# Kernel tuning notes

Measured on AMD Instinct MI355X. Metric: run time of the kernel, lower is better.

The kernel has to match this reference:

```python
import jax, jax.numpy as jnp
import numpy as np

TAU = 32.0


def setup_inputs() -> dict:
    key = jax.random.key(0)
    k1, k2, k3, k4, k5 = jax.random.split(key, 5)
    B, IN, E, D, M = 32768, 768, 256, 9, 10
    feature = jax.random.normal(k1, (B, IN), dtype=jnp.float32)
    category = jax.random.randint(k2, (B,), 0, D)  # unused in forward math
    # nn.Linear(input_dim, emb_dim, bias=False) stores weight [emb_dim, input_dim]
    W_topic = jax.random.normal(k3, (E, IN), dtype=jnp.float32) * (1.0 / np.sqrt(IN))
    W_domain = jax.random.normal(k4, (E, IN), dtype=jnp.float32) * (1.0 / np.sqrt(IN))
    memory = jax.random.normal(k5, (D, M, E), dtype=jnp.float32)  # stacked domain memory banks
    return {"feature": feature, "category": category, "W_topic": W_topic,
            "W_domain": W_domain, "memory": memory}


def reference(feature, category, W_topic, W_domain, memory):
    # L2-normalize features along dim 1
    f = feature / jnp.linalg.norm(feature, axis=1, keepdims=True)
    topic = f @ W_topic.T      # [B, E]
    dom = f @ W_domain.T       # [B, E]
    # per-domain memory attention, batched over all D domains at once
    att = jax.nn.softmax(jnp.einsum('be,dme->bdm', topic, memory) * TAU, axis=-1)  # [B, D, M]
    sep = jnp.einsum('bdm,dme->bde', att, memory)                                   # [B, D, E]
    domain_att = jnp.einsum('bde,be->bd', sep, dom)                                 # [B, D]
    return jax.nn.softmax(domain_att * TAU, axis=1)[:, None, :]                     # [B, 1, D]
```

## Files before the change

kernel.cpp:

```cpp
#include <hip/hip_runtime.h>
#include <math.h>

typedef __attribute__((ext_vector_type(8))) short short8;
typedef __attribute__((ext_vector_type(4))) float f32x4;
typedef __attribute__((ext_vector_type(4))) unsigned short u16x4;

#define TAUF 32.0f

constexpr int NT     = 24;
constexpr int BUF_SZ = 40960;
constexpr int A_HI   = 0;
constexpr int A_LO   = 8192;
constexpr int B_HI   = 16384;
constexpr int B_LO   = 28672;
constexpr int CSTR   = 196;

__global__ __launch_bounds__(256) void precompute_pr(
    const float* __restrict__ Wt, const float* __restrict__ Wd,
    const float* __restrict__ mem, unsigned short* __restrict__ PRhi,
    unsigned short* __restrict__ PRlo) {
  int blk = blockIdx.x, t = threadIdx.x;
  if (blk >= 180) {
    for (int p = 0; p < 3; ++p) {
      PRhi[blk * 768 + t + p * 256] = 0;
      PRlo[blk * 768 + t + p * 256] = 0;
    }
    return;
  }
  __shared__ float mlds[256];
  const float* W = (blk >= 90) ? Wd : Wt;
  int dm = (blk >= 90) ? blk - 90 : blk;
  mlds[t] = mem[dm * 256 + t];
  __syncthreads();
  for (int p = 0; p < 3; ++p) {
    int i = t + p * 256;
    float acc = 0.f;
    #pragma unroll 8
    for (int e = 0; e < 256; ++e) acc += mlds[e] * W[e * 768 + i];
    unsigned int b = __float_as_uint(acc);
    unsigned short hi = (unsigned short)(b >> 16);
    float hf = __uint_as_float(b & 0xffff0000u);
    unsigned short lo = (unsigned short)(__float_as_uint(acc - hf) >> 16);
    PRhi[blk * 768 + i] = hi;
    PRlo[blk * 768 + i] = lo;
  }
}

__global__ __launch_bounds__(512, 1) void fused_mfma(
    const float* __restrict__ feat, const unsigned short* __restrict__ PRhi,
    const unsigned short* __restrict__ PRlo, float* __restrict__ out) {
  __shared__ f32x4 smemv[6400];
  __shared__ float invn[128];
  __shared__ float sarr[1152];
  char* smem = (char*)smemv;

  const int t    = threadIdx.x;
  const int lane = t & 63;
  const int wid  = t >> 6;
  const int rg   = wid >> 1;
  const int cg   = wid & 1;
  const int b0   = blockIdx.x * 128;

  const int ar0 = t >> 3;
  const int aq  = t & 7;
  const float* gA0 = feat + (size_t)(b0 + ar0) * 768 + aq * 4;
  const float* gA1 = gA0 + (size_t)64 * 768;
  const int aw0 = ar0 * 64 + aq * 8;
  const int aw1 = (ar0 + 64) * 64 + aq * 8;

  const int iid = wid * 3;

  const int laneA = ((lane & 15) << 6) | ((lane >> 4) << 4);

  f32x4 acc0[6], acc1[6];
  #pragma unroll
  for (int j = 0; j < 6; ++j) {
    acc0[j] = (f32x4){0.f, 0.f, 0.f, 0.f};
    acc1[j] = (f32x4){0.f, 0.f, 0.f, 0.f};
  }
  float ssq0 = 0.f, ssq1 = 0.f;

  auto issueB = [&](int kt, int bb) {
    #pragma unroll
    for (int u = 0; u < 3; ++u) {
      int i  = iid + u;
      int pl = i / 12;
      int idx = i - pl * 12;
      int G  = idx * 64 + lane;
      const unsigned short* basep = pl ? PRlo : PRhi;
      const char* g = (const char*)basep + (G >> 2) * 1536 + kt * 64 + (G & 3) * 16;
      char* l = smem + bb * BUF_SZ + (pl ? B_LO : B_HI) + idx * 1024;
      __builtin_amdgcn_global_load_lds((const unsigned int*)g, (unsigned int*)l,
                                       16, 0, 0);
    }
  };

  auto cvtwrite = [&](float4 v, char* dhi, char* dlo, float& ssq) {
    ssq += v.x * v.x + v.y * v.y + v.z * v.z + v.w * v.w;
    float xs[4] = {v.x, v.y, v.z, v.w};
    u16x4 hi, lo;
    #pragma unroll
    for (int e = 0; e < 4; ++e) {
      float x = xs[e];
      unsigned int bu = __float_as_uint(x);
      hi[e] = (unsigned short)(bu >> 16);
      float hf = __uint_as_float(bu & 0xffff0000u);
      lo[e] = (unsigned short)(__float_as_uint(x - hf) >> 16);
    }
    *(u16x4*)dhi = hi;
    *(u16x4*)dlo = lo;
  };

  auto domfma = [&](int bb) {
    char* base = smem + bb * BUF_SZ;
    const int aoff = rg * 2048 + laneA;
    short8 ah0 = *(const short8*)(base + A_HI + aoff);
    short8 ah1 = *(const short8*)(base + A_HI + aoff + 1024);
    short8 al0 = *(const short8*)(base + A_LO + aoff);
    short8 al1 = *(const short8*)(base + A_LO + aoff + 1024);
    const int boff = cg * 6144 + laneA;
    #pragma unroll
    for (int j = 0; j < 6; ++j) {
      short8 bh = *(const short8*)(base + B_HI + boff + j * 1024);
      short8 bl = *(const short8*)(base + B_LO + boff + j * 1024);
      acc0[j] = __builtin_amdgcn_mfma_f32_16x16x32_bf16(ah0, bh, acc0[j], 0, 0, 0);
      acc0[j] = __builtin_amdgcn_mfma_f32_16x16x32_bf16(al0, bh, acc0[j], 0, 0, 0);
      acc0[j] = __builtin_amdgcn_mfma_f32_16x16x32_bf16(ah0, bl, acc0[j], 0, 0, 0);
      acc1[j] = __builtin_amdgcn_mfma_f32_16x16x32_bf16(ah1, bh, acc1[j], 0, 0, 0);
      acc1[j] = __builtin_amdgcn_mfma_f32_16x16x32_bf16(al1, bh, acc1[j], 0, 0, 0);
      acc1[j] = __builtin_amdgcn_mfma_f32_16x16x32_bf16(ah1, bl, acc1[j], 0, 0, 0);
    }
  };

  float4 sa0 = *(const float4*)gA0;
  float4 sa1 = *(const float4*)gA1;
  issueB(0, 0);
  cvtwrite(sa0, smem + A_HI + aw0, smem + A_LO + aw0, ssq0);
  cvtwrite(sa1, smem + A_HI + aw1, smem + A_LO + aw1, ssq1);
  float4 sb0 = *(const float4*)(gA0 + 32);
  float4 sb1 = *(const float4*)(gA1 + 32);
  __syncthreads();

  for (int kp = 0; kp < 11; ++kp) {
    int kt = 2 * kp;
    issueB(kt + 1, 1);
    cvtwrite(sb0, smem + BUF_SZ + A_HI + aw0, smem + BUF_SZ + A_LO + aw0, ssq0);
    cvtwrite(sb1, smem + BUF_SZ + A_HI + aw1, smem + BUF_SZ + A_LO + aw1, ssq1);
    sa0 = *(const float4*)(gA0 + (kt + 2) * 32);
    sa1 = *(const float4*)(gA1 + (kt + 2) * 32);
    domfma(0);
    __syncthreads();
    issueB(kt + 2, 0);
    cvtwrite(sa0, smem + A_HI + aw0, smem + A_LO + aw0, ssq0);
    cvtwrite(sa1, smem + A_HI + aw1, smem + A_LO + aw1, ssq1);
    sb0 = *(const float4*)(gA0 + (kt + 3) * 32);
    sb1 = *(const float4*)(gA1 + (kt + 3) * 32);
    domfma(1);
    __syncthreads();
  }
  issueB(23, 1);
  cvtwrite(sb0, smem + BUF_SZ + A_HI + aw0, smem + BUF_SZ + A_LO + aw0, ssq0);
  cvtwrite(sb1, smem + BUF_SZ + A_HI + aw1, smem + BUF_SZ + A_LO + aw1, ssq1);
  domfma(0);
  __syncthreads();
  domfma(1);

  float s0 = ssq0, s1 = ssq1;
  #pragma unroll
  for (int m = 1; m <= 4; m <<= 1) {
    s0 += __shfl_xor(s0, m, 64);
    s1 += __shfl_xor(s1, m, 64);
  }
  if ((t & 7) == 0) {
    invn[ar0]      = rsqrtf(s0);
    invn[ar0 + 64] = rsqrtf(s1);
  }
  __syncthreads();

  float* Clds = (float*)smem;
  #pragma unroll
  for (int rt = 0; rt < 2; ++rt) {
    int rbase = rg * 32 + rt * 16 + ((lane >> 4) << 2);
    #pragma unroll
    for (int j = 0; j < 6; ++j) {
      int col = (cg * 6 + j) * 16 + (lane & 15);
      f32x4 v = rt ? acc1[j] : acc0[j];
      #pragma unroll
      for (int jj = 0; jj < 4; ++jj)
        Clds[(rbase + jj) * CSTR + col] = v[jj] * invn[rbase + jj];
    }
  }
  __syncthreads();

  for (int pid = t; pid < 1152; pid += 512) {
    int row = pid / 9, d = pid - row * 9;
    const float* qp = Clds + row * CSTR + d * 10;
    const float* rp = qp + 90;
    float mx = qp[0];
    #pragma unroll
    for (int m = 1; m < 10; ++m) mx = fmaxf(mx, qp[m]);
    float s = 0.f, val = 0.f;
    #pragma unroll
    for (int m = 0; m < 10; ++m) {
      float e = __expf(TAUF * (qp[m] - mx));
      s += e;
      val += e * rp[m];
    }
    sarr[pid] = val / s;
  }
  __syncthreads();

  if (t < 128) {
    float v[9];
    #pragma unroll
    for (int d = 0; d < 9; ++d) v[d] = sarr[t * 9 + d];
    float mx = v[0];
    #pragma unroll
    for (int d = 1; d < 9; ++d) mx = fmaxf(mx, v[d]);
    float s = 0.f;
    float e[9];
    #pragma unroll
    for (int d = 0; d < 9; ++d) {
      e[d] = __expf(TAUF * (v[d] - mx));
      s += e[d];
    }
    float is = 1.f / s;
    #pragma unroll
    for (int d = 0; d < 9; ++d)
      out[(size_t)(b0 + t) * 9 + d] = e[d] * is;
  }
}

extern "C" void kernel_launch(void* const* d_in, const int* in_sizes, int n_in,
                              void* d_out, int out_size, void* d_ws, size_t ws_size,
                              hipStream_t stream) {
  const float* feat = (const float*)d_in[0];
  const float* Wt  = (const float*)d_in[2];
  const float* Wd  = (const float*)d_in[3];
  const float* mem = (const float*)d_in[4];
  float* outp = (float*)d_out;

  unsigned short* PRhi = (unsigned short*)d_ws;
  unsigned short* PRlo = PRhi + 192 * 768;

  precompute_pr<<<192, 256, 0, stream>>>(Wt, Wd, mem, PRhi, PRlo);
  const int B = in_sizes[1];
  fused_mfma<<<B / 128, 512, 0, stream>>>(feat, PRhi, PRlo, outp);
}
```

Before: 75.15 us.

## Halve fused block to 64 rows with 256 threads, two blocks per CU

The fused MFMA kernel now processes 64 batch rows per 256-thread block instead of 128 rows per 512 threads. It uses a new k-major LDS layout for A and B and a smaller 64KB double buffer, which allows two blocks per CU. The B staging from the PR workspace is reloaded per block, doubling total PR traffic, and the row-norm reduction now goes through LDS instead of shuffles. The precompute kernel is also vectorized to float4 loads with 192 threads per block.

```diff
diff --git a/kernel.cpp b/kernel.cpp
--- a/kernel.cpp
+++ b/kernel.cpp
@@ -4,54 +4,61 @@
 typedef __attribute__((ext_vector_type(8))) short short8;
 typedef __attribute__((ext_vector_type(4))) float f32x4;
 typedef __attribute__((ext_vector_type(4))) unsigned short u16x4;
+typedef __attribute__((ext_vector_type(8))) unsigned short u16x8;
 
 #define TAUF 32.0f
 
-constexpr int NT     = 24;
-constexpr int BUF_SZ = 40960;
 constexpr int A_HI   = 0;
-constexpr int A_LO   = 8192;
-constexpr int B_HI   = 16384;
-constexpr int B_LO   = 28672;
+constexpr int A_LO   = 4096;
+constexpr int B_HI   = 8192;
+constexpr int B_LO   = 20480;
+constexpr int BUF_SZ = 32768;
 constexpr int CSTR   = 196;
 
-__global__ __launch_bounds__(256) void precompute_pr(
+__global__ __launch_bounds__(192) void precompute_pr(
     const float* __restrict__ Wt, const float* __restrict__ Wd,
     const float* __restrict__ mem, unsigned short* __restrict__ PRhi,
     unsigned short* __restrict__ PRlo) {
   int blk = blockIdx.x, t = threadIdx.x;
+  int i0 = t * 4;
   if (blk >= 180) {
-    for (int p = 0; p < 3; ++p) {
-      PRhi[blk * 768 + t + p * 256] = 0;
-      PRlo[blk * 768 + t + p * 256] = 0;
-    }
+    u16x4 z = {0, 0, 0, 0};
+    *(u16x4*)&PRhi[blk * 768 + i0] = z;
+    *(u16x4*)&PRlo[blk * 768 + i0] = z;
     return;
   }
   __shared__ float mlds[256];
   const float* W = (blk >= 90) ? Wd : Wt;
   int dm = (blk >= 90) ? blk - 90 : blk;
-  mlds[t] = mem[dm * 256 + t];
-  __syncthreads();
-  for (int p = 0; p < 3; ++p) {
-    int i = t + p * 256;
-    float acc = 0.f;
-    #pragma unroll 8
-    for (int e = 0; e < 256; ++e) acc += mlds[e] * W[e * 768 + i];
-    unsigned int b = __float_as_uint(acc);
-    unsigned short hi = (unsigned short)(b >> 16);
-    float hf = __uint_as_float(b & 0xffff0000u);
-    unsigned short lo = (unsigned short)(__float_as_uint(acc - hf) >> 16);
-    PRhi[blk * 768 + i] = hi;
-    PRlo[blk * 768 + i] = lo;
-  }
+  for (int i = t; i < 256; i += 192) mlds[i] = mem[dm * 256 + i];
+  __syncthreads();
+  float ax = 0.f, ay = 0.f, az = 0.f, aw = 0.f;
+  #pragma unroll 8
+  for (int e = 0; e < 256; ++e) {
+    float m = mlds[e];
+    float4 w = *(const float4*)&W[e * 768 + i0];
+    ax += m * w.x; ay += m * w.y; az += m * w.z; aw += m * w.w;
+  }
+  float xs[4] = {ax, ay, az, aw};
+  u16x4 hi, lo;
+  #pragma unroll
+  for (int e = 0; e < 4; ++e) {
+    unsigned int bu = __float_as_uint(xs[e]);
+    hi[e] = (unsigned short)(bu >> 16);
+    float hf = __uint_as_float(bu & 0xffff0000u);
+    lo[e] = (unsigned short)(__float_as_uint(xs[e] - hf) >> 16);
+  }
+  *(u16x4*)&PRhi[blk * 768 + i0] = hi;
+  *(u16x4*)&PRlo[blk * 768 + i0] = lo;
 }
 
-__global__ __launch_bounds__(512, 1) void fused_mfma(
+__global__ __launch_bounds__(256, 2) void fused_mfma(
     const float* __restrict__ feat, const unsigned short* __restrict__ PRhi,
     const unsigned short* __restrict__ PRlo, float* __restrict__ out) {
-  __shared__ f32x4 smemv[6400];
-  __shared__ float invn[128];
-  __shared__ float sarr[1152];
+  __shared__ f32x4 smemv[4096];
+  __shared__ float ssql[256];
+  __shared__ float invn[64];
+  __shared__ float sarr[576];
   char* smem = (char*)smemv;
 
   const int t    = threadIdx.x;
@@ -59,18 +66,14 @@
   const int wid  = t >> 6;
   const int rg   = wid >> 1;
   const int cg   = wid & 1;
-  const int b0   = blockIdx.x * 128;
-
-  const int ar0 = t >> 3;
-  const int aq  = t & 7;
-  const float* gA0 = feat + (size_t)(b0 + ar0) * 768 + aq * 4;
-  const float* gA1 = gA0 + (size_t)64 * 768;
-  const int aw0 = ar0 * 64 + aq * 8;
-  const int aw1 = (ar0 + 64) * 64 + aq * 8;
-
-  const int iid = wid * 3;
-
-  const int laneA = ((lane & 15) << 6) | ((lane >> 4) << 4);
+  const int b0   = blockIdx.x * 64;
+
+  const int arow = t & 63;
+  const int ag   = t >> 6;
+  const float* gA = feat + (size_t)(b0 + arow) * 768 + ag * 8;
+  const int awr  = ag * 1024 + arow * 16;
+
+  const int iid = wid * 6;
 
   f32x4 acc0[6], acc1[6];
   #pragma unroll
@@ -78,51 +81,53 @@
     acc0[j] = (f32x4){0.f, 0.f, 0.f, 0.f};
     acc1[j] = (f32x4){0.f, 0.f, 0.f, 0.f};
   }
-  float ssq0 = 0.f, ssq1 = 0.f;
+  float ssq = 0.f;
 
   auto issueB = [&](int kt, int bb) {
     #pragma unroll
-    for (int u = 0; u < 3; ++u) {
-      int i  = iid + u;
-      int pl = i / 12;
+    for (int u = 0; u < 6; ++u) {
+      int i   = iid + u;
+      int pl  = i / 12;
       int idx = i - pl * 12;
-      int G  = idx * 64 + lane;
+      int g   = idx & 3;
+      int c0  = (idx >> 2) << 6;
       const unsigned short* basep = pl ? PRlo : PRhi;
-      const char* g = (const char*)basep + (G >> 2) * 1536 + kt * 64 + (G & 3) * 16;
-      char* l = smem + bb * BUF_SZ + (pl ? B_LO : B_HI) + idx * 1024;
-      __builtin_amdgcn_global_load_lds((const unsigned int*)g, (unsigned int*)l,
-                                       16, 0, 0);
+      const char* gg = (const char*)basep + (size_t)(c0 + lane) * 1536 +
+                       kt * 64 + g * 16;
+      char* l = smem + bb * BUF_SZ + (pl ? B_LO : B_HI) + g * 3072 + c0 * 16;
+      __builtin_amdgcn_global_load_lds((const unsigned int*)gg,
+                                       (unsigned int*)l, 16, 0, 0);
     }
   };
 
-  auto cvtwrite = [&](float4 v, char* dhi, char* dlo, float& ssq) {
-    ssq += v.x * v.x + v.y * v.y + v.z * v.z + v.w * v.w;
-    float xs[4] = {v.x, v.y, v.z, v.w};
-    u16x4 hi, lo;
-    #pragma unroll
-    for (int e = 0; e < 4; ++e) {
+  auto cvt8 = [&](float4 a, float4 b, char* dhi, char* dlo) {
+    float xs[8] = {a.x, a.y, a.z, a.w, b.x, b.y, b.z, b.w};
+    u16x8 hi, lo;
+    #pragma unroll
+    for (int e = 0; e < 8; ++e) {
       float x = xs[e];
+      ssq += x * x;
       unsigned int bu = __float_as_uint(x);
       hi[e] = (unsigned short)(bu >> 16);
       float hf = __uint_as_float(bu & 0xffff0000u);
       lo[e] = (unsigned short)(__float_as_uint(x - hf) >> 16);
     }
-    *(u16x4*)dhi = hi;
-    *(u16x4*)dlo = lo;
+    *(u16x8*)dhi = hi;
+    *(u16x8*)dlo = lo;
   };
 
   auto domfma = [&](int bb) {
     char* base = smem + bb * BUF_SZ;
-    const int aoff = rg * 2048 + laneA;
-    short8 ah0 = *(const short8*)(base + A_HI + aoff);
-    short8 ah1 = *(const short8*)(base + A_HI + aoff + 1024);
-    short8 al0 = *(const short8*)(base + A_LO + aoff);
-    short8 al1 = *(const short8*)(base + A_LO + aoff + 1024);
-    const int boff = cg * 6144 + laneA;
+    const int la = ((lane >> 4) << 10) | ((lane & 15) << 4);
+    short8 ah0 = *(const short8*)(base + A_HI + rg * 512 + la);
+    short8 ah1 = *(const short8*)(base + A_HI + rg * 512 + 256 + la);
+    short8 al0 = *(const short8*)(base + A_LO + rg * 512 + la);
+    short8 al1 = *(const short8*)(base + A_LO + rg * 512 + 256 + la);
+    const int lb = (lane >> 4) * 3072 + cg * 1536 + ((lane & 15) << 4);
     #pragma unroll
     for (int j = 0; j < 6; ++j) {
-      short8 bh = *(const short8*)(base + B_HI + boff + j * 1024);
-      short8 bl = *(const short8*)(base + B_LO + boff + j * 1024);
+      short8 bh = *(const short8*)(base + B_HI + lb + j * 256);
+      short8 bl = *(const short8*)(base + B_LO + lb + j * 256);
       acc0[j] = __builtin_amdgcn_mfma_f32_16x16x32_bf16(ah0, bh, acc0[j], 0, 0, 0);
       acc0[j] = __builtin_amdgcn_mfma_f32_16x16x32_bf16(al0, bh, acc0[j], 0, 0, 0);
       acc0[j] = __builtin_amdgcn_mfma_f32_16x16x32_bf16(ah0, bl, acc0[j], 0, 0, 0);
@@ -132,49 +137,39 @@
     }
   };
 
-  float4 sa0 = *(const float4*)gA0;
-  float4 sa1 = *(const float4*)gA1;
+  float4 sa0 = *(const float4*)gA;
+  float4 sa1 = *(const float4*)(gA + 4);
   issueB(0, 0);
-  cvtwrite(sa0, smem + A_HI + aw0, smem + A_LO + aw0, ssq0);
-  cvtwrite(sa1, smem + A_HI + aw1, smem + A_LO + aw1, ssq1);
-  float4 sb0 = *(const float4*)(gA0 + 32);
-  float4 sb1 = *(const float4*)(gA1 + 32);
+  cvt8(sa0, sa1, smem + A_HI + awr, smem + A_LO + awr);
+  float4 sb0 = *(const float4*)(gA + 32);
+  float4 sb1 = *(const float4*)(gA + 36);
   __syncthreads();
 
   for (int kp = 0; kp < 11; ++kp) {
     int kt = 2 * kp;
     issueB(kt + 1, 1);
-    cvtwrite(sb0, smem + BUF_SZ + A_HI + aw0, smem + BUF_SZ + A_LO + aw0, ssq0);
-    cvtwrite(sb1, smem + BUF_SZ + A_HI + aw1, smem + BUF_SZ + A_LO + aw1, ssq1);
-    sa0 = *(const float4*)(gA0 + (kt + 2) * 32);
-    sa1 = *(const float4*)(gA1 + (kt + 2) * 32);
+    cvt8(sb0, sb1, smem + BUF_SZ + A_HI + awr, smem + BUF_SZ + A_LO + awr);
+    sa0 = *(const float4*)(gA + (kt + 2) * 32);
+    sa1 = *(const float4*)(gA + (kt + 2) * 32 + 4);
     domfma(0);
     __syncthreads();
     issueB(kt + 2, 0);
-    cvtwrite(sa0, smem + A_HI + aw0, smem + A_LO + aw0, ssq0);
-    cvtwrite(sa1, smem + A_HI + aw1, smem + A_LO + aw1, ssq1);
-    sb0 = *(const float4*)(gA0 + (kt + 3) * 32);
-    sb1 = *(const float4*)(gA1 + (kt + 3) * 32);
+    cvt8(sa0, sa1, smem + A_HI + awr, smem + A_LO + awr);
+    sb0 = *(const float4*)(gA + (kt + 3) * 32);
+    sb1 = *(const float4*)(gA + (kt + 3) * 32 + 4);
     domfma(1);
     __syncthreads();
   }
   issueB(23, 1);
-  cvtwrite(sb0, smem + BUF_SZ + A_HI + aw0, smem + BUF_SZ + A_LO + aw0, ssq0);
-  cvtwrite(sb1, smem + BUF_SZ + A_HI + aw1, smem + BUF_SZ + A_LO + aw1, ssq1);
+  cvt8(sb0, sb1, smem + BUF_SZ + A_HI + awr, smem + BUF_SZ + A_LO + awr);
   domfma(0);
   __syncthreads();
   domfma(1);
 
-  float s0 = ssq0, s1 = ssq1;
-  #pragma unroll
-  for (int m = 1; m <= 4; m <<= 1) {
-    s0 += __shfl_xor(s0, m, 64);
-    s1 += __shfl_xor(s1, m, 64);
-  }
-  if ((t & 7) == 0) {
-    invn[ar0]      = rsqrtf(s0);
-    invn[ar0 + 64] = rsqrtf(s1);
-  }
+  ssql[t] = ssq;
+  __syncthreads();
+  if (t < 64)
+    invn[t] = rsqrtf(ssql[t] + ssql[t + 64] + ssql[t + 128] + ssql[t + 192]);
   __syncthreads();
 
   float* Clds = (float*)smem;
@@ -183,7 +178,7 @@
     int rbase = rg * 32 + rt * 16 + ((lane >> 4) << 2);
     #pragma unroll
     for (int j = 0; j < 6; ++j) {
-      int col = (cg * 6 + j) * 16 + (lane & 15);
+      int col = cg * 96 + j * 16 + (lane & 15);
       f32x4 v = rt ? acc1[j] : acc0[j];
       #pragma unroll
       for (int jj = 0; jj < 4; ++jj)
@@ -192,7 +187,7 @@
   }
   __syncthreads();
 
-  for (int pid = t; pid < 1152; pid += 512) {
+  for (int pid = t; pid < 576; pid += 256) {
     int row = pid / 9, d = pid - row * 9;
     const float* qp = Clds + row * CSTR + d * 10;
     const float* rp = qp + 90;
@@ -210,7 +205,7 @@
   }
   __syncthreads();
 
-  if (t < 128) {
+  if (t < 64) {
     float v[9];
     #pragma unroll
     for (int d = 0; d < 9; ++d) v[d] = sarr[t * 9 + d];
@@ -243,7 +238,7 @@
   unsigned short* PRhi = (unsigned short*)d_ws;
   unsigned short* PRlo = PRhi + 192 * 768;
 
-  precompute_pr<<<192, 256, 0, stream>>>(Wt, Wd, mem, PRhi, PRlo);
+  precompute_pr<<<192, 192, 0, stream>>>(Wt, Wd, mem, PRhi, PRlo);
   const int B = in_sizes[1];
-  fused_mfma<<<B / 128, 512, 0, stream>>>(feat, PRhi, PRlo, outp);
+  fused_mfma<<<B / 64, 256, 0, stream>>>(feat, PRhi, PRlo, outp);
 }
```

Result: slower. 94.57 us (+25.8%).
